# Performance work log

Hardware: AMD Instinct MI355X
Metric: run time of the kernel (lower is better)

Reference implementation:

```python
import jax, jax.numpy as jnp
import numpy as np

B, D_K, D_V = 1024, 64, 64
N_FEAT, RANK, K = 32768, 1, 32

def _normalize(a):
    return a / jnp.linalg.norm(a, axis=-1, keepdims=True)

def setup_inputs() -> dict:
    key = jax.random.key(0)
    k0, k1, k2, k3, k4 = jax.random.split(key, 5)
    x = jax.random.normal(k0, (B, D_K, D_V), dtype=jnp.float32)
    V_enc = _normalize(jax.random.normal(k1, (N_FEAT, RANK, D_K), dtype=jnp.float32))
    W_enc = _normalize(jax.random.normal(k2, (N_FEAT, RANK, D_V), dtype=jnp.float32))
    V_dec = _normalize(jax.random.normal(k3, (N_FEAT, RANK, D_K), dtype=jnp.float32))
    W_dec = _normalize(jax.random.normal(k4, (N_FEAT, RANK, D_V), dtype=jnp.float32))
    b_enc = jnp.zeros((N_FEAT,), dtype=jnp.float32)
    bias = jnp.zeros((D_K, D_V), dtype=jnp.float32)
    return {"x": x, "V_enc": V_enc, "W_enc": W_enc, "b_enc": b_enc,
            "V_dec": V_dec, "W_dec": W_dec, "bias": bias}

def reference(x, V_enc, W_enc, b_enc, V_dec, W_dec, bias):
    b, d_k, d_v = x.shape
    n_feat = V_enc.shape[0]
    x_flat = x.reshape(b, d_k * d_v)
    # encode: einsum('irk,bkv,irv->bi') == x_flat @ (sum_r v_ir (x) w_ir)^T
    M_enc = jnp.einsum('irk,irv->ikv', V_enc, W_enc).reshape(n_feat, d_k * d_v)
    pre = x_flat @ M_enc.T + b_enc                       # [B, n_feat]
    # topk activation with relu on the kept values, zeros elsewhere
    vals, idx = jax.lax.top_k(pre, K)                    # [B, K]
    vals = jnp.maximum(vals, 0.0)
    coeffs = jnp.zeros_like(pre).at[jnp.arange(b)[:, None], idx].set(vals)
    # decode: einsum('bi,irk,irv->bkv')
    M_dec = jnp.einsum('irk,irv->ikv', V_dec, W_dec).reshape(n_feat, d_k * d_v)
    recon_flat = coeffs @ M_dec + bias.reshape(-1)
    recon = recon_flat.reshape(b, d_k, d_v)
    mse = jnp.mean((recon_flat - x_flat) ** 2)
    # fresh steps_since_active buffer (zeros) + dead_threshold=100 -> no dead
    # features, so aux_loss == 0 exactly; total loss == mse.
    return recon, coeffs, mse
```

## Files before the change

### kernel.cpp

```cpp
#include <hip/hip_runtime.h>
#include <hip/hip_bf16.h>
#include <hip/hip_fp8.h>
#include <stdint.h>

#define NFEAT 32768
#define BATCH 1024
#define DK 64
#define DV 64
#define DD 4096
#define KSEL 32
#define CAND_CAP 512
#define CAND_TARGET 128

using bf16 = __bf16;
using bf16x8 = __attribute__((ext_vector_type(8))) __bf16;
using f32x4 = __attribute__((ext_vector_type(4))) float;
using f32x16 = __attribute__((ext_vector_type(16))) float;
using i32x4 = __attribute__((ext_vector_type(4))) int;
using i32x8 = __attribute__((ext_vector_type(8))) int;

__device__ __forceinline__ void gload_lds16(const void* g, void* l) {
  __builtin_amdgcn_global_load_lds((const __attribute__((address_space(1))) void*)g,
                                   (__attribute__((address_space(3))) void*)l,
                                   16, 0, 0);
}

__device__ inline unsigned mono16(unsigned u) {
  return (u & 0x8000u) ? ((~u) & 0xFFFFu) : (u | 0x8000u);
}

__global__ void k_convert_x(const float* __restrict__ x, unsigned char* __restrict__ xb, int n) {
  int i = (blockIdx.x * blockDim.x + threadIdx.x) * 16;
  if (i >= n) return;
  union { unsigned char b[16]; uint4 u; } o;
#pragma unroll
  for (int j = 0; j < 16; j += 4) {
    float4 v = *reinterpret_cast<const float4*>(x + i + j);
    o.b[j + 0] = __hip_fp8_e4m3(v.x).__x;
    o.b[j + 1] = __hip_fp8_e4m3(v.y).__x;
    o.b[j + 2] = __hip_fp8_e4m3(v.z).__x;
    o.b[j + 3] = __hip_fp8_e4m3(v.w).__x;
  }
  *reinterpret_cast<uint4*>(xb + i) = o.u;
}

__global__ void k_build_menc(const float* __restrict__ Venc, const float* __restrict__ Wenc,
                             unsigned char* __restrict__ Menc) {
  int i = blockIdx.x;
  int t = threadIdx.x;
  int k = t >> 2;
  int vb = (t & 3) << 4;
  float vk = 16.0f * Venc[i * DK + k];
  const float* wrow = Wenc + i * DV + vb;
  union { unsigned char b[16]; uint4 u; } o;
#pragma unroll
  for (int j = 0; j < 16; j += 4) {
    float4 w = *reinterpret_cast<const float4*>(wrow + j);
    o.b[j + 0] = __hip_fp8_e4m3(vk * w.x).__x;
    o.b[j + 1] = __hip_fp8_e4m3(vk * w.y).__x;
    o.b[j + 2] = __hip_fp8_e4m3(vk * w.z).__x;
    o.b[j + 3] = __hip_fp8_e4m3(vk * w.w).__x;
  }
  *reinterpret_cast<uint4*>(Menc + (size_t)i * DD + (t << 4)) = o.u;
}

#define BM 256
#define BN 256
#define BKB 128
#define NT (DD / BKB)
#define ABUF 32768
#define BUFSZ 65536
#define GEMM_LDS (2 * BUFSZ)

__device__ __forceinline__ void stage_chunk(const unsigned char* __restrict__ G, size_t rowbase,
                                            int kb0, int c, int lane, char* dstbase) {
  const unsigned char* src = G + (rowbase + (size_t)(c * 8 + (lane >> 3))) * DD + kb0 +
                             (((lane & 7) ^ (lane >> 3)) << 4);
  gload_lds16(src, dstbase + c * 1024);
}

__device__ __forceinline__ i32x8 frag_ld8(const char* base, int row, int col) {
  i32x4 lo = *reinterpret_cast<const i32x4*>(base + row * 128 + (col ^ ((row & 7) << 4)));
  i32x4 hi = *reinterpret_cast<const i32x4*>(base + row * 128 + ((col + 16) ^ ((row & 7) << 4)));
  i32x8 r;
  r[0] = lo[0]; r[1] = lo[1]; r[2] = lo[2]; r[3] = lo[3];
  r[4] = hi[0]; r[5] = hi[1]; r[6] = hi[2]; r[7] = hi[3];
  return r;
}

__device__ __forceinline__ int chA(int half, int idx) {
  return (idx < 8 ? idx : idx + 8) + half * 8;
}
__device__ __forceinline__ int chB(int half, int idx) {
  return (idx >> 2) * 8 + (idx & 3) + half * 4;
}

#define LD_A(H)                                                                     \
  _Pragma("unroll") for (int mb = 0; mb < 2; ++mb)                                  \
  _Pragma("unroll") for (int kh = 0; kh < 2; ++kh)                                  \
    afr[mb][kh] = frag_ld8(cur, wr * 128 + (H) * 64 + mb * 32 + (lane & 31),        \
                           kh * 64 + ((lane >> 5) << 5));

#define LD_B(H)                                                                     \
  _Pragma("unroll") for (int kh = 0; kh < 2; ++kh)                                  \
    bfr[(H)][kh] = frag_ld8(cur + ABUF, wc * 64 + (H) * 32 + (lane & 31),           \
                            kh * 64 + ((lane >> 5) << 5));

#define ST_A(HALF, KT)                                                              \
  stage_chunk(A, brow, (KT) * BKB, chA(HALF, wave * 2), lane, nxt);                 \
  stage_chunk(A, brow, (KT) * BKB, chA(HALF, wave * 2 + 1), lane, nxt);

#define ST_B(HALF, KT)                                                              \
  stage_chunk(Bt, bcol, (KT) * BKB, chB(HALF, wave * 2), lane, nxt + ABUF);         \
  stage_chunk(Bt, bcol, (KT) * BKB, chB(HALF, wave * 2 + 1), lane, nxt + ABUF);

#define MFMA_Q(MH, NB)                                                              \
  asm volatile("s_waitcnt lgkmcnt(0)" ::: "memory");                                \
  __builtin_amdgcn_sched_barrier(0);                                                \
  __builtin_amdgcn_s_setprio(1);                                                    \
  _Pragma("unroll") for (int mb = 0; mb < 2; ++mb)                                  \
  _Pragma("unroll") for (int kh = 0; kh < 2; ++kh)                                  \
    acc[(MH) * 2 + mb][NB] = __builtin_amdgcn_mfma_scale_f32_32x32x64_f8f6f4(       \
        afr[mb][kh], bfr[NB][kh], acc[(MH) * 2 + mb][NB], 0, 0, 0, 0x7F, 0, 0x7F);  \
  __builtin_amdgcn_s_setprio(0);

#define VMC(N) asm volatile("s_waitcnt vmcnt(" #N ")" ::: "memory");
#define LGKM0 asm volatile("s_waitcnt lgkmcnt(0)" ::: "memory");
#define BARR                                                                        \
  asm volatile("s_barrier" ::: "memory");                                           \
  __builtin_amdgcn_sched_barrier(0);

__global__ __launch_bounds__(512, 2)
void k_gemm(const unsigned char* __restrict__ A, const unsigned char* __restrict__ Bt,
            const float* __restrict__ benc, bf16* __restrict__ C) {
  extern __shared__ char lds[];
  int tid = threadIdx.x;
  int wave = tid >> 6;
  int lane = tid & 63;
  int wr = wave >> 2;
  int wc = wave & 3;

  int d = blockIdx.x;
  int lw = (d & 7) * 64 + (d >> 3);
  int q = lw >> 2;
  int p = lw & 3;
  size_t brow = (size_t)p * BM;
  size_t bcol = (size_t)q * BN;

  f32x16 acc[4][2] = {};
  i32x8 afr[2][2];
  i32x8 bfr[2][2];

  {
    char* nxt = lds;
    ST_B(0, 0) ST_A(0, 0) ST_B(1, 0) ST_A(1, 0)
  }
  VMC(4)
  BARR

#pragma unroll 1
  for (int u = 0; u < NT - 1; ++u) {
    char* cur = lds + (u & 1) * BUFSZ;
    char* nxt = lds + ((u + 1) & 1) * BUFSZ;
    int k1 = u + 1;
    LD_A(0) LD_B(0)
    ST_B(0, k1)
    VMC(4)
    BARR
    MFMA_Q(0, 0)
    LD_B(1)
    ST_A(0, k1)
    VMC(4)
    BARR
    MFMA_Q(0, 1)
    LD_A(1)
    ST_B(1, k1) ST_A(1, k1)
    VMC(4)
    LGKM0
    BARR
    MFMA_Q(1, 1)
    MFMA_Q(1, 0)
  }

  {
    char* cur = lds + ((NT - 1) & 1) * BUFSZ;
    LD_A(0) LD_B(0)
    VMC(2)
    BARR
    MFMA_Q(0, 0)
    LD_B(1)
    VMC(0)
    BARR
    MFMA_Q(0, 1)
    LD_A(1)
    LGKM0
    BARR
    MFMA_Q(1, 1)
    MFMA_Q(1, 0)
  }

#pragma unroll
  for (int nb = 0; nb < 2; ++nb) {
    size_t col = bcol + wc * 64 + nb * 32 + (lane & 31);
    float be = benc[col];
#pragma unroll
    for (int MB = 0; MB < 4; ++MB) {
      size_t row0 = brow + wr * 128 + MB * 32 + ((lane >> 5) << 2);
#pragma unroll
      for (int reg = 0; reg < 16; ++reg) {
        size_t row = row0 + (reg & 3) + ((reg >> 2) << 3);
        C[row * NFEAT + col] = (bf16)(acc[MB][nb][reg] * 0.0625f + be);
      }
    }
  }
}

__global__ void k_topk(const unsigned short* __restrict__ pre, int* __restrict__ cand_idx,
                       int* __restrict__ cand_cnt) {
  __shared__ int hist[8192];
  __shared__ int csum[256];
  __shared__ int sBstar;
  __shared__ int scount;
  int b = blockIdx.x;
  int t = threadIdx.x;
  const unsigned short* row = pre + (size_t)b * NFEAT;
  for (int i = t; i < 8192; i += 256) hist[i] = 0;
  if (t == 0) scount = 0;
  __syncthreads();

  for (int i = (t << 3); i < NFEAT; i += 2048) {
    uint4 v = *reinterpret_cast<const uint4*>(row + i);
#pragma unroll
    for (int j = 0; j < 4; ++j) {
      unsigned w = (&v.x)[j];
      atomicAdd(&hist[mono16(w & 0xFFFFu) >> 3], 1);
      atomicAdd(&hist[mono16(w >> 16) >> 3], 1);
    }
  }
  __syncthreads();

  int s = 0;
  for (int i = 0; i < 32; ++i) s += hist[t * 32 + i];
  csum[t] = s;
  __syncthreads();
  int suff = 0;
  for (int j = t + 1; j < 256; ++j) suff += csum[j];
  if (suff < CAND_TARGET && suff + s >= CAND_TARGET) {
    int acc = suff;
    int bstar = t * 32;
    for (int i = 31; i >= 0; --i) {
      acc += hist[t * 32 + i];
      if (acc >= CAND_TARGET) { bstar = t * 32 + i; break; }
    }
    sBstar = bstar;
  }
  __syncthreads();
  int Bstar = sBstar;
  int* cidx = cand_idx + b * CAND_CAP;

  for (int i = (t << 3); i < NFEAT; i += 2048) {
    uint4 v = *reinterpret_cast<const uint4*>(row + i);
#pragma unroll
    for (int j = 0; j < 4; ++j) {
      unsigned w = (&v.x)[j];
      int b0 = (int)(mono16(w & 0xFFFFu) >> 3);
      int b1 = (int)(mono16(w >> 16) >> 3);
      if (b0 >= Bstar) { int p2 = atomicAdd(&scount, 1); if (p2 < CAND_CAP) cidx[p2] = i + j * 2; }
      if (b1 >= Bstar) { int p2 = atomicAdd(&scount, 1); if (p2 < CAND_CAP) cidx[p2] = i + j * 2 + 1; }
    }
  }
  __syncthreads();
  if (t == 0) cand_cnt[b] = (scount < CAND_CAP) ? scount : CAND_CAP;
}

__global__ void k_refine(const float* __restrict__ x,
                         const float* __restrict__ Venc,
                         const float* __restrict__ Wenc,
                         const float* __restrict__ benc,
                         const float* __restrict__ Vdec,
                         const float* __restrict__ Wdec,
                         const float* __restrict__ bias,
                         const int* __restrict__ cand_idx,
                         const int* __restrict__ cand_cnt,
                         float* __restrict__ recon,
                         float* __restrict__ coeffs,
                         float* __restrict__ msepart) {
  __shared__ float rval[CAND_CAP];
  __shared__ int ridx[CAND_CAP];
  __shared__ float selv[KSEL];
  __shared__ int seli[KSEL];
  __shared__ float Vd[KSEL][DK];
  __shared__ float Wd[KSEL][DV];
  __shared__ float red[256];

  int b = blockIdx.x;
  int t = threadIdx.x;
  int wave = t >> 6;
  int lane = t & 63;

  const float* xr = x + (size_t)b * DD;

  float xreg[DK];
#pragma unroll
  for (int kk = 0; kk < DK; ++kk)
    xreg[kk] = xr[kk * DV + lane];

  int c = cand_cnt[b];
  if (c > CAND_CAP) c = CAND_CAP;
  for (int i = t; i < c; i += 256) ridx[i] = cand_idx[b * CAND_CAP + i];
  __syncthreads();

  for (int j = wave; j < c; j += 4) {
    int fi = __builtin_amdgcn_readfirstlane(ridx[j]);
    const float* vr = Venc + (size_t)fi * DK;
    float w = Wenc[(size_t)fi * DV + lane];
    float a0 = 0.f, a1 = 0.f, a2 = 0.f, a3 = 0.f;
#pragma unroll
    for (int kk = 0; kk < DK; kk += 4) {
      a0 = fmaf(xreg[kk + 0], vr[kk + 0], a0);
      a1 = fmaf(xreg[kk + 1], vr[kk + 1], a1);
      a2 = fmaf(xreg[kk + 2], vr[kk + 2], a2);
      a3 = fmaf(xreg[kk + 3], vr[kk + 3], a3);
    }
    float p2 = ((a0 + a1) + (a2 + a3)) * w;
#pragma unroll
    for (int off = 1; off < 64; off <<= 1) p2 += __shfl_xor(p2, off);
    if (lane == 0) rval[j] = p2 + benc[fi];
  }
  __syncthreads();

  for (int t2 = t; t2 < c; t2 += 256) {
    float v = rval[t2];
    int fi = ridx[t2];
    int rank = 0;
    for (int j = 0; j < c; ++j) {
      float vj = rval[j];
      if (vj > v || (vj == v && ridx[j] < fi)) ++rank;
    }
    if (rank < KSEL) { selv[rank] = v; seli[rank] = fi; }
  }
  __syncthreads();

  if (t < KSEL) {
    float v = fmaxf(selv[t], 0.f);
    selv[t] = v;
    coeffs[(size_t)b * NFEAT + seli[t]] = v;
  }
  __syncthreads();

  for (int i = t; i < KSEL * DK; i += 256) {
    int s = i >> 6, e = i & 63;
    Vd[s][e] = Vdec[(size_t)seli[s] * DK + e];
    Wd[s][e] = Wdec[(size_t)seli[s] * DV + e];
  }
  __syncthreads();

  int k = t >> 2;
  int vb = (t & 3) << 4;
  float4 r4[4];
#pragma unroll
  for (int g = 0; g < 4; ++g)
    r4[g] = *reinterpret_cast<const float4*>(bias + k * DV + vb + g * 4);
#pragma unroll
  for (int s = 0; s < KSEL; ++s) {
    float a = selv[s] * Vd[s][k];
    const float4* wrow = reinterpret_cast<const float4*>(&Wd[s][vb]);
#pragma unroll
    for (int g = 0; g < 4; ++g) {
      float4 wv = wrow[g];
      r4[g].x = fmaf(a, wv.x, r4[g].x);
      r4[g].y = fmaf(a, wv.y, r4[g].y);
      r4[g].z = fmaf(a, wv.z, r4[g].z);
      r4[g].w = fmaf(a, wv.w, r4[g].w);
    }
  }
  float m = 0.f;
  float* ro = recon + (size_t)b * DD + k * DV + vb;
#pragma unroll
  for (int g = 0; g < 4; ++g) {
    float4 xv = *reinterpret_cast<const float4*>(xr + k * DV + vb + g * 4);
    float dx = r4[g].x - xv.x, dy = r4[g].y - xv.y;
    float dz = r4[g].z - xv.z, dw = r4[g].w - xv.w;
    m = fmaf(dx, dx, m); m = fmaf(dy, dy, m);
    m = fmaf(dz, dz, m); m = fmaf(dw, dw, m);
    *reinterpret_cast<float4*>(ro + g * 4) = r4[g];
  }
  red[t] = m;
  __syncthreads();
  for (int s2 = 128; s2 > 0; s2 >>= 1) {
    if (t < s2) red[t] += red[t + s2];
    __syncthreads();
  }
  if (t == 0) msepart[b] = red[0];
}

__global__ void k_mse(const float* __restrict__ msepart, float* __restrict__ out) {
  __shared__ float red[256];
  int t = threadIdx.x;
  float s = 0.f;
  for (int i = t; i < BATCH; i += 256) s += msepart[i];
  red[t] = s;
  __syncthreads();
  for (int k = 128; k > 0; k >>= 1) {
    if (t < k) red[t] += red[t + k];
    __syncthreads();
  }
  if (t == 0) out[0] = red[0] / (float)((size_t)BATCH * DD);
}

extern "C" void kernel_launch(void* const* d_in, const int* in_sizes, int n_in,
                              void* d_out, int out_size, void* d_ws, size_t ws_size,
                              hipStream_t stream) {
  const float* x    = (const float*)d_in[0];
  const float* Venc = (const float*)d_in[1];
  const float* Wenc = (const float*)d_in[2];
  const float* benc = (const float*)d_in[3];
  const float* Vdec = (const float*)d_in[4];
  const float* Wdec = (const float*)d_in[5];
  const float* bias = (const float*)d_in[6];

  float* out = (float*)d_out;
  float* recon  = out;
  float* coeffs = out + (size_t)BATCH * DD;
  float* mse    = coeffs + (size_t)BATCH * NFEAT;

  char* wsp = (char*)d_ws;
  unsigned char* xb8 = (unsigned char*)wsp;   wsp += (size_t)BATCH * DD;
  unsigned char* Menc8 = (unsigned char*)wsp; wsp += (size_t)NFEAT * DD;
  int* cand_idx = (int*)wsp;                  wsp += (size_t)BATCH * CAND_CAP * sizeof(int);
  int* cand_cnt = (int*)wsp;                  wsp += (size_t)BATCH * sizeof(int);
  float* msepart = (float*)wsp;               wsp += (size_t)BATCH * sizeof(float);

  bf16* pre = (bf16*)coeffs;

  hipFuncSetAttribute((const void*)k_gemm, hipFuncAttributeMaxDynamicSharedMemorySize,
                      GEMM_LDS);

  k_convert_x<<<(BATCH * DD) / (256 * 16), 256, 0, stream>>>(x, xb8, BATCH * DD);
  k_build_menc<<<NFEAT, 256, 0, stream>>>(Venc, Wenc, Menc8);
  k_gemm<<<(BATCH / BM) * (NFEAT / BN), 512, GEMM_LDS, stream>>>(xb8, Menc8, benc, pre);
  k_topk<<<BATCH, 256, 0, stream>>>((const unsigned short*)pre, cand_idx, cand_cnt);
  hipMemsetAsync(coeffs, 0, (size_t)BATCH * NFEAT * sizeof(float), stream);
  k_refine<<<BATCH, 256, 0, stream>>>(x, Venc, Wenc, benc, Vdec, Wdec, bias,
                                      cand_idx, cand_cnt, recon, coeffs, msepart);
  k_mse<<<1, 256, 0, stream>>>(msepart, mse);
}
```

Measured before the change: 309.2 us.

## Use MFMA-fragment-ordered LDS layout and fuse coeffs zeroing into topk

```diff
diff --git a/kernel.cpp b/kernel.cpp
--- a/kernel.cpp
+++ b/kernel.cpp
@@ -74,14 +74,16 @@
 
 __device__ __forceinline__ void stage_chunk(const unsigned char* __restrict__ G, size_t rowbase,
                                             int kb0, int c, int lane, char* dstbase) {
-  const unsigned char* src = G + (rowbase + (size_t)(c * 8 + (lane >> 3))) * DD + kb0 +
-                             (((lane & 7) ^ (lane >> 3)) << 4);
+  int b32 = c >> 2, kg = c & 3;
+  const unsigned char* src = G + (rowbase + (size_t)(b32 * 32 + (lane & 31))) * DD + kb0 +
+                             kg * 32 + ((lane >> 5) << 4);
   gload_lds16(src, dstbase + c * 1024);
 }
 
-__device__ __forceinline__ i32x8 frag_ld8(const char* base, int row, int col) {
-  i32x4 lo = *reinterpret_cast<const i32x4*>(base + row * 128 + (col ^ ((row & 7) << 4)));
-  i32x4 hi = *reinterpret_cast<const i32x4*>(base + row * 128 + ((col + 16) ^ ((row & 7) << 4)));
+__device__ __forceinline__ i32x8 frag_ld8(const char* base, int chunk, int lane) {
+  const char* p = base + chunk * 1024 + (lane & 31) * 16;
+  i32x4 lo = *reinterpret_cast<const i32x4*>(p);
+  i32x4 hi = *reinterpret_cast<const i32x4*>(p + 512);
   i32x8 r;
   r[0] = lo[0]; r[1] = lo[1]; r[2] = lo[2]; r[3] = lo[3];
   r[4] = hi[0]; r[5] = hi[1]; r[6] = hi[2]; r[7] = hi[3];
@@ -89,22 +91,23 @@
 }
 
 __device__ __forceinline__ int chA(int half, int idx) {
-  return (idx < 8 ? idx : idx + 8) + half * 8;
+  int g = idx >> 2, kg = idx & 3;
+  int mb32 = (g & 1) + ((g >> 1) << 2) + half * 2;
+  return mb32 * 4 + kg;
 }
 __device__ __forceinline__ int chB(int half, int idx) {
-  return (idx >> 2) * 8 + (idx & 3) + half * 4;
+  int nb32 = ((idx >> 2) << 1) + half;
+  return nb32 * 4 + (idx & 3);
 }
 
 #define LD_A(H)                                                                     \
   _Pragma("unroll") for (int mb = 0; mb < 2; ++mb)                                  \
   _Pragma("unroll") for (int kh = 0; kh < 2; ++kh)                                  \
-    afr[mb][kh] = frag_ld8(cur, wr * 128 + (H) * 64 + mb * 32 + (lane & 31),        \
-                           kh * 64 + ((lane >> 5) << 5));
+    afr[mb][kh] = frag_ld8(cur, (wr * 4 + (H) * 2 + mb) * 4 + kh * 2 + (lane >> 5), lane);
 
 #define LD_B(H)                                                                     \
   _Pragma("unroll") for (int kh = 0; kh < 2; ++kh)                                  \
-    bfr[(H)][kh] = frag_ld8(cur + ABUF, wc * 64 + (H) * 32 + (lane & 31),           \
-                            kh * 64 + ((lane >> 5) << 5));
+    bfr[(H)][kh] = frag_ld8(cur + ABUF, (wc * 2 + (H)) * 4 + kh * 2 + (lane >> 5), lane);
 
 #define ST_A(HALF, KT)                                                              \
   stage_chunk(A, brow, (KT) * BKB, chA(HALF, wave * 2), lane, nxt);                 \
@@ -216,7 +219,7 @@
 }
 
 __global__ void k_topk(const unsigned short* __restrict__ pre, int* __restrict__ cand_idx,
-                       int* __restrict__ cand_cnt) {
+                       int* __restrict__ cand_cnt, float* __restrict__ coeffs) {
   __shared__ int hist[8192];
   __shared__ int csum[256];
   __shared__ int sBstar;
@@ -271,6 +274,11 @@
   }
   __syncthreads();
   if (t == 0) cand_cnt[b] = (scount < CAND_CAP) ? scount : CAND_CAP;
+
+  float* crow = coeffs + (size_t)b * NFEAT;
+  float4 z4 = {0.f, 0.f, 0.f, 0.f};
+  for (int i = (t << 2); i < NFEAT; i += 1024)
+    *reinterpret_cast<float4*>(crow + i) = z4;
 }
 
 __global__ void k_refine(const float* __restrict__ x,
@@ -430,8 +438,7 @@
   int* cand_idx = (int*)wsp;                  wsp += (size_t)BATCH * CAND_CAP * sizeof(int);
   int* cand_cnt = (int*)wsp;                  wsp += (size_t)BATCH * sizeof(int);
   float* msepart = (float*)wsp;               wsp += (size_t)BATCH * sizeof(float);
-
-  bf16* pre = (bf16*)coeffs;
+  bf16* pre = (bf16*)wsp;                     wsp += (size_t)BATCH * NFEAT * sizeof(bf16);
 
   hipFuncSetAttribute((const void*)k_gemm, hipFuncAttributeMaxDynamicSharedMemorySize,
                       GEMM_LDS);
@@ -439,8 +446,7 @@
   k_convert_x<<<(BATCH * DD) / (256 * 16), 256, 0, stream>>>(x, xb8, BATCH * DD);
   k_build_menc<<<NFEAT, 256, 0, stream>>>(Venc, Wenc, Menc8);
   k_gemm<<<(BATCH / BM) * (NFEAT / BN), 512, GEMM_LDS, stream>>>(xb8, Menc8, benc, pre);
-  k_topk<<<BATCH, 256, 0, stream>>>((const unsigned short*)pre, cand_idx, cand_cnt);
-  hipMemsetAsync(coeffs, 0, (size_t)BATCH * NFEAT * sizeof(float), stream);
+  k_topk<<<BATCH, 256, 0, stream>>>((const unsigned short*)pre, cand_idx, cand_cnt, coeffs);
   k_refine<<<BATCH, 256, 0, stream>>>(x, Venc, Wenc, benc, Vdec, Wdec, bias,
                                       cand_idx, cand_cnt, recon, coeffs, msepart);
   k_mse<<<1, 256, 0, stream>>>(msepart, mse);
```

New measurement: 315.7 us. +2.1%, slower.
